# Kernel optimization log

Measured on AMD Instinct MI355X. Metric: run time of the kernel, lower is better.

Reference implementation:

```python
import jax, jax.numpy as jnp
import numpy as np

VOCAB, D, E, TOP_K, B, S = 32000, 1024, 16, 2, 2048, 128
H = 2 * D  # expert hidden
LN_EPS = 1e-5


def setup_inputs() -> dict:
    key = jax.random.key(0)
    ks = jax.random.split(key, 12)
    sd = 0.02
    return {
        "x": jax.random.randint(ks[0], (B, S), 0, VOCAB),
        "embed": jax.random.normal(ks[1], (VOCAB, D), jnp.float32) * sd,
        "gate_w": jax.random.normal(ks[2], (D, E), jnp.float32) * sd,
        "gate_b": jnp.zeros((E,), jnp.float32),
        "w1": jax.random.normal(ks[3], (E, D, H), jnp.float32) * sd,
        "b1": jnp.zeros((E, H), jnp.float32),
        "w2": jax.random.normal(ks[4], (E, H, D), jnp.float32) * sd,
        "b2": jnp.zeros((E, D), jnp.float32),
        "ln_g": jnp.ones((D,), jnp.float32),
        "ln_b": jnp.zeros((D,), jnp.float32),
        "head_w": jax.random.normal(ks[5], (D, 20), jnp.float32) * sd,
        "head_b": jnp.zeros((20,), jnp.float32),
    }


def reference(x, embed, gate_w, gate_b, w1, b1, w2, b2, ln_g, ln_b, head_w, head_b):
    # embed mean-pool: [B,S,D] -> [B,D]
    h = jnp.mean(embed[x], axis=1)
    # gate + top-k routing
    scores = jax.nn.softmax(h @ gate_w + gate_b, axis=-1)  # [B,E]
    topk_vals, topk_idx = jax.lax.top_k(scores, TOP_K)     # [B,K]
    # combine weights per (token, expert): sum of topk vals routed to e
    comb_w = jnp.sum(topk_vals[:, :, None] * jax.nn.one_hot(topk_idx, E, dtype=h.dtype), axis=1)  # [B,E]
    # dense all-expert MLP (same math as per-token dispatch), weighted combine
    pre = jnp.einsum('bd,edh->beh', h, w1) + b1            # [B,E,H]
    ye = jnp.einsum('beh,ehd->bed', jax.nn.relu(pre), w2) + b2  # [B,E,D]
    combined = jnp.einsum('be,bed->bd', comb_w, ye)        # [B,D]
    # LayerNorm + head
    mu = jnp.mean(combined, axis=-1, keepdims=True)
    var = jnp.mean(jnp.square(combined - mu), axis=-1, keepdims=True)
    normed = (combined - mu) * jax.lax.rsqrt(var + LN_EPS) * ln_g + ln_b
    logits = normed @ head_w + head_b                      # [B,20]
    return logits, topk_idx
```

## Files before the change

kernel.cpp:

```cpp
#include <hip/hip_runtime.h>
#include <math.h>

#define B_TOK 2048
#define SEQ   128
#define D_DIM 1024
#define E_NUM 16
#define H_DIM 2048

#define TM 128
#define TN 64
#define KT 32
#define A_LD 40

typedef __attribute__((ext_vector_type(8))) short short8;
typedef __attribute__((ext_vector_type(4))) float f32x4;

__device__ __forceinline__ float bf2f(unsigned short h) {
  return __uint_as_float(((unsigned)h) << 16);
}

__device__ __forceinline__ void split2(float x, unsigned short& hi, unsigned short& lo) {
  unsigned u = __float_as_uint(x);
  hi = (unsigned short)(u >> 16);
  float lof = x - __uint_as_float(u & 0xFFFF0000u);
  lo = (unsigned short)(__float_as_uint(lof) >> 16);
}

__global__ __launch_bounds__(256) void k_embed_mean(const int* __restrict__ x,
                                                    const float* __restrict__ embed,
                                                    unsigned short* __restrict__ h_hi,
                                                    unsigned short* __restrict__ h_lo) {
  const int b = blockIdx.x;
  const int t = threadIdx.x;
  __shared__ int sx[SEQ];
  if (t < SEQ) sx[t] = x[b * SEQ + t];
  __syncthreads();
  float4 acc = make_float4(0.f, 0.f, 0.f, 0.f);
  const int col = t * 4;
  for (int s = 0; s < SEQ; ++s) {
    const float4 v = *reinterpret_cast<const float4*>(embed + (size_t)sx[s] * D_DIM + col);
    acc.x += v.x; acc.y += v.y; acc.z += v.z; acc.w += v.w;
  }
  const float inv = 1.0f / (float)SEQ;
  float vv[4] = {acc.x * inv, acc.y * inv, acc.z * inv, acc.w * inv};
  ushort4 hv, lv;
  split2(vv[0], hv.x, lv.x); split2(vv[1], hv.y, lv.y);
  split2(vv[2], hv.z, lv.z); split2(vv[3], hv.w, lv.w);
  *reinterpret_cast<ushort4*>(h_hi + (size_t)b * D_DIM + col) = hv;
  *reinterpret_cast<ushort4*>(h_lo + (size_t)b * D_DIM + col) = lv;
}

__global__ __launch_bounds__(64) void k_gate(const unsigned short* __restrict__ h_hi,
                                             const unsigned short* __restrict__ h_lo,
                                             const float* __restrict__ gate_w,
                                             const float* __restrict__ gate_b,
                                             int* __restrict__ counts,
                                             int* __restrict__ lists,
                                             float* __restrict__ wlist,
                                             float* __restrict__ out_idx) {
  const int b = blockIdx.x;
  const int l = threadIdx.x;
  float z[E_NUM];
#pragma unroll
  for (int e = 0; e < E_NUM; ++e) z[e] = 0.f;
  const size_t base = (size_t)b * D_DIM;
  for (int d = l; d < D_DIM; d += 64) {
    const float hv = bf2f(h_hi[base + d]) + bf2f(h_lo[base + d]);
    const float* gw = gate_w + d * E_NUM;
#pragma unroll
    for (int e = 0; e < E_NUM; ++e) z[e] = fmaf(hv, gw[e], z[e]);
  }
#pragma unroll
  for (int e = 0; e < E_NUM; ++e) {
    float v = z[e];
#pragma unroll
    for (int off = 32; off >= 1; off >>= 1) v += __shfl_xor(v, off, 64);
    z[e] = v;
  }
  if (l == 0) {
#pragma unroll
    for (int e = 0; e < E_NUM; ++e) z[e] += gate_b[e];
    float mx = z[0];
#pragma unroll
    for (int e = 1; e < E_NUM; ++e) mx = fmaxf(mx, z[e]);
    float p[E_NUM];
    float se = 0.f;
#pragma unroll
    for (int e = 0; e < E_NUM; ++e) { p[e] = expf(z[e] - mx); se += p[e]; }
    const float invs = 1.0f / se;
    int e1 = 0; float z1 = z[0];
#pragma unroll
    for (int e = 1; e < E_NUM; ++e) if (z[e] > z1) { z1 = z[e]; e1 = e; }
    int e2 = -1; float z2 = -1e30f;
#pragma unroll
    for (int e = 0; e < E_NUM; ++e) if (e != e1 && z[e] > z2) { z2 = z[e]; e2 = e; }
    const float w1v = p[e1] * invs;
    const float w2v = p[e2] * invs;
    const int pos1 = atomicAdd(&counts[e1], 1);
    lists[e1 * B_TOK + pos1] = b * 2 + 0;
    wlist[e1 * B_TOK + pos1] = w1v;
    const int pos2 = atomicAdd(&counts[e2], 1);
    lists[e2 * B_TOK + pos2] = b * 2 + 1;
    wlist[e2 * B_TOK + pos2] = w2v;
    out_idx[b * 2 + 0] = (float)e1;
    out_idx[b * 2 + 1] = (float)e2;
  }
}

__global__ __launch_bounds__(256) void k_gemm1(const unsigned short* __restrict__ a_hi,
                                               const unsigned short* __restrict__ a_lo,
                                               const float* __restrict__ w1,
                                               const float* __restrict__ b1,
                                               const int* __restrict__ counts,
                                               const int* __restrict__ lists,
                                               unsigned short* __restrict__ act_hi,
                                               unsigned short* __restrict__ act_lo) {
  const int e = blockIdx.z;
  const int n_e = counts[e];
  const int m0 = blockIdx.y * TM;
  if (m0 >= n_e) return;
  const int n0 = blockIdx.x * TN;
  const int* lst = lists + e * B_TOK;

  __shared__ short AsH[TM][A_LD];
  __shared__ short AsL[TM][A_LD];
  __shared__ short BsH[TN][A_LD];
  __shared__ short BsL[TN][A_LD];

  const int tid = threadIdx.x;
  const int r0 = tid >> 3;
  const int sl = tid & 7;
  const int spart = sl & 3;
  const unsigned short* abase = (sl < 4) ? a_hi : a_lo;
  short* lds_a = (sl < 4) ? &AsH[0][0] : &AsL[0][0];
  size_t arowoff[4];
#pragma unroll
  for (int p = 0; p < 4; ++p) {
    const int m = m0 + p * 32 + r0;
    const int ent = lst[(m < n_e) ? m : 0];
    arowoff[p] = (size_t)(ent >> 1) * D_DIM;
  }
  const int bn = tid & 63;
  const int bkq = tid >> 6;
  const float* bcol = w1 + (size_t)e * D_DIM * H_DIM + n0 + bn;

  const int wv = tid >> 6;
  const int lane = tid & 63;
  const int fm = lane & 15;
  const int fq = lane >> 4;
  const int mrow = wv * 32;
  f32x4 acc[2][4];
#pragma unroll
  for (int mi = 0; mi < 2; ++mi)
#pragma unroll
    for (int ni = 0; ni < 4; ++ni) acc[mi][ni] = (f32x4){0.f, 0.f, 0.f, 0.f};

  for (int kb = 0; kb < D_DIM; kb += KT) {
#pragma unroll
    for (int p = 0; p < 4; ++p) {
      const int4 v = *reinterpret_cast<const int4*>(abase + arowoff[p] + kb + 8 * spart);
      *reinterpret_cast<int4*>(lds_a + (p * 32 + r0) * A_LD + 8 * spart) = v;
    }
    {
      unsigned u[8];
      float f[8];
#pragma unroll
      for (int j = 0; j < 8; ++j) {
        f[j] = bcol[(size_t)(kb + bkq * 8 + j) * H_DIM];
        u[j] = __float_as_uint(f[j]);
      }
      int4 hv, lv;
      unsigned lw[8];
#pragma unroll
      for (int j = 0; j < 8; ++j) {
        const float lof = f[j] - __uint_as_float(u[j] & 0xFFFF0000u);
        lw[j] = __float_as_uint(lof);
      }
      hv.x = (int)((u[0] >> 16) | (u[1] & 0xFFFF0000u));
      hv.y = (int)((u[2] >> 16) | (u[3] & 0xFFFF0000u));
      hv.z = (int)((u[4] >> 16) | (u[5] & 0xFFFF0000u));
      hv.w = (int)((u[6] >> 16) | (u[7] & 0xFFFF0000u));
      lv.x = (int)((lw[0] >> 16) | (lw[1] & 0xFFFF0000u));
      lv.y = (int)((lw[2] >> 16) | (lw[3] & 0xFFFF0000u));
      lv.z = (int)((lw[4] >> 16) | (lw[5] & 0xFFFF0000u));
      lv.w = (int)((lw[6] >> 16) | (lw[7] & 0xFFFF0000u));
      *reinterpret_cast<int4*>(&BsH[bn][bkq * 8]) = hv;
      *reinterpret_cast<int4*>(&BsL[bn][bkq * 8]) = lv;
    }
    __syncthreads();
    short8 aH[2], aL[2], bH[4], bL[4];
#pragma unroll
    for (int mi = 0; mi < 2; ++mi) {
      aH[mi] = *reinterpret_cast<const short8*>(&AsH[mrow + mi * 16 + fm][fq * 8]);
      aL[mi] = *reinterpret_cast<const short8*>(&AsL[mrow + mi * 16 + fm][fq * 8]);
    }
#pragma unroll
    for (int ni = 0; ni < 4; ++ni) {
      bH[ni] = *reinterpret_cast<const short8*>(&BsH[ni * 16 + fm][fq * 8]);
      bL[ni] = *reinterpret_cast<const short8*>(&BsL[ni * 16 + fm][fq * 8]);
    }
#pragma unroll
    for (int mi = 0; mi < 2; ++mi)
#pragma unroll
      for (int ni = 0; ni < 4; ++ni) {
        acc[mi][ni] = __builtin_amdgcn_mfma_f32_16x16x32_bf16(aH[mi], bH[ni], acc[mi][ni], 0, 0, 0);
        acc[mi][ni] = __builtin_amdgcn_mfma_f32_16x16x32_bf16(aH[mi], bL[ni], acc[mi][ni], 0, 0, 0);
        acc[mi][ni] = __builtin_amdgcn_mfma_f32_16x16x32_bf16(aL[mi], bH[ni], acc[mi][ni], 0, 0, 0);
      }
    __syncthreads();
  }
  float bz[4];
#pragma unroll
  for (int ni = 0; ni < 4; ++ni) bz[ni] = b1[(size_t)e * H_DIM + n0 + ni * 16 + fm];
#pragma unroll
  for (int mi = 0; mi < 2; ++mi) {
#pragma unroll
    for (int r = 0; r < 4; ++r) {
      const int m = m0 + mrow + mi * 16 + fq * 4 + r;
      if (m < n_e) {
        const int ent = lst[m];
        unsigned short* oh = act_hi + (size_t)ent * H_DIM + n0 + fm;
        unsigned short* ol = act_lo + (size_t)ent * H_DIM + n0 + fm;
#pragma unroll
        for (int ni = 0; ni < 4; ++ni) {
          float v = fmaxf(acc[mi][ni][r] + bz[ni], 0.f);
          unsigned short hh, ll;
          split2(v, hh, ll);
          oh[ni * 16] = hh;
          ol[ni * 16] = ll;
        }
      }
    }
  }
}

__global__ __launch_bounds__(256) void k_gemm2(const unsigned short* __restrict__ a_hi,
                                               const unsigned short* __restrict__ a_lo,
                                               const float* __restrict__ w2,
                                               const float* __restrict__ b2,
                                               const int* __restrict__ counts,
                                               const int* __restrict__ lists,
                                               const float* __restrict__ wlist,
                                               float* __restrict__ combined) {
  const int e = blockIdx.z;
  const int n_e = counts[e];
  const int m0 = blockIdx.y * TM;
  if (m0 >= n_e) return;
  const int n0 = blockIdx.x * TN;
  const int* lst = lists + e * B_TOK;

  __shared__ short AsH[TM][A_LD];
  __shared__ short AsL[TM][A_LD];
  __shared__ short BsH[TN][A_LD];
  __shared__ short BsL[TN][A_LD];

  const int tid = threadIdx.x;
  const int r0 = tid >> 3;
  const int sl = tid & 7;
  const int spart = sl & 3;
  const unsigned short* abase = (sl < 4) ? a_hi : a_lo;
  short* lds_a = (sl < 4) ? &AsH[0][0] : &AsL[0][0];
  size_t arowoff[4];
#pragma unroll
  for (int p = 0; p < 4; ++p) {
    const int m = m0 + p * 32 + r0;
    const int ent = lst[(m < n_e) ? m : 0];
    arowoff[p] = (size_t)ent * H_DIM;
  }
  const int bn = tid & 63;
  const int bkq = tid >> 6;
  const float* bcol = w2 + (size_t)e * H_DIM * D_DIM + n0 + bn;

  const int wv = tid >> 6;
  const int lane = tid & 63;
  const int fm = lane & 15;
  const int fq = lane >> 4;
  const int mrow = wv * 32;
  f32x4 acc[2][4];
#pragma unroll
  for (int mi = 0; mi < 2; ++mi)
#pragma unroll
    for (int ni = 0; ni < 4; ++ni) acc[mi][ni] = (f32x4){0.f, 0.f, 0.f, 0.f};

  for (int kb = 0; kb < H_DIM; kb += KT) {
#pragma unroll
    for (int p = 0; p < 4; ++p) {
      const int4 v = *reinterpret_cast<const int4*>(abase + arowoff[p] + kb + 8 * spart);
      *reinterpret_cast<int4*>(lds_a + (p * 32 + r0) * A_LD + 8 * spart) = v;
    }
    {
      unsigned u[8];
      float f[8];
#pragma unroll
      for (int j = 0; j < 8; ++j) {
        f[j] = bcol[(size_t)(kb + bkq * 8 + j) * D_DIM];
        u[j] = __float_as_uint(f[j]);
      }
      int4 hv, lv;
      unsigned lw[8];
#pragma unroll
      for (int j = 0; j < 8; ++j) {
        const float lof = f[j] - __uint_as_float(u[j] & 0xFFFF0000u);
        lw[j] = __float_as_uint(lof);
      }
      hv.x = (int)((u[0] >> 16) | (u[1] & 0xFFFF0000u));
      hv.y = (int)((u[2] >> 16) | (u[3] & 0xFFFF0000u));
      hv.z = (int)((u[4] >> 16) | (u[5] & 0xFFFF0000u));
      hv.w = (int)((u[6] >> 16) | (u[7] & 0xFFFF0000u));
      lv.x = (int)((lw[0] >> 16) | (lw[1] & 0xFFFF0000u));
      lv.y = (int)((lw[2] >> 16) | (lw[3] & 0xFFFF0000u));
      lv.z = (int)((lw[4] >> 16) | (lw[5] & 0xFFFF0000u));
      lv.w = (int)((lw[6] >> 16) | (lw[7] & 0xFFFF0000u));
      *reinterpret_cast<int4*>(&BsH[bn][bkq * 8]) = hv;
      *reinterpret_cast<int4*>(&BsL[bn][bkq * 8]) = lv;
    }
    __syncthreads();
    short8 aH[2], aL[2], bH[4], bL[4];
#pragma unroll
    for (int mi = 0; mi < 2; ++mi) {
      aH[mi] = *reinterpret_cast<const short8*>(&AsH[mrow + mi * 16 + fm][fq * 8]);
      aL[mi] = *reinterpret_cast<const short8*>(&AsL[mrow + mi * 16 + fm][fq * 8]);
    }
#pragma unroll
    for (int ni = 0; ni < 4; ++ni) {
      bH[ni] = *reinterpret_cast<const short8*>(&BsH[ni * 16 + fm][fq * 8]);
      bL[ni] = *reinterpret_cast<const short8*>(&BsL[ni * 16 + fm][fq * 8]);
    }
#pragma unroll
    for (int mi = 0; mi < 2; ++mi)
#pragma unroll
      for (int ni = 0; ni < 4; ++ni) {
        acc[mi][ni] = __builtin_amdgcn_mfma_f32_16x16x32_bf16(aH[mi], bH[ni], acc[mi][ni], 0, 0, 0);
        acc[mi][ni] = __builtin_amdgcn_mfma_f32_16x16x32_bf16(aH[mi], bL[ni], acc[mi][ni], 0, 0, 0);
        acc[mi][ni] = __builtin_amdgcn_mfma_f32_16x16x32_bf16(aL[mi], bH[ni], acc[mi][ni], 0, 0, 0);
      }
    __syncthreads();
  }
  float bz[4];
#pragma unroll
  for (int ni = 0; ni < 4; ++ni) bz[ni] = b2[(size_t)e * D_DIM + n0 + ni * 16 + fm];
#pragma unroll
  for (int mi = 0; mi < 2; ++mi) {
#pragma unroll
    for (int r = 0; r < 4; ++r) {
      const int m = m0 + mrow + mi * 16 + fq * 4 + r;
      if (m < n_e) {
        const int ent = lst[m];
        const float w = wlist[e * B_TOK + m];
        float* dst = combined + (size_t)(ent >> 1) * D_DIM + n0 + fm;
#pragma unroll
        for (int ni = 0; ni < 4; ++ni) {
          atomicAdd(&dst[ni * 16], w * (acc[mi][ni][r] + bz[ni]));
        }
      }
    }
  }
}

__global__ __launch_bounds__(256) void k_ln_head(const float* __restrict__ combined,
                                                 const float* __restrict__ ln_g,
                                                 const float* __restrict__ ln_b,
                                                 const float* __restrict__ head_w,
                                                 const float* __restrict__ head_b,
                                                 float* __restrict__ logits) {
  const int b = blockIdx.x;
  const int t = threadIdx.x;
  const int lane = t & 63, wid = t >> 6;
  __shared__ float red[8];
  __shared__ float pr[4][20];
  const int d0 = t * 4;
  const float4 v = *reinterpret_cast<const float4*>(combined + (size_t)b * D_DIM + d0);
  float s = v.x + v.y + v.z + v.w;
#pragma unroll
  for (int off = 32; off >= 1; off >>= 1) s += __shfl_xor(s, off, 64);
  if (lane == 0) red[wid] = s;
  __syncthreads();
  const float mu = (red[0] + red[1] + red[2] + red[3]) * (1.0f / D_DIM);
  const float dx = v.x - mu, dy = v.y - mu, dz = v.z - mu, dw = v.w - mu;
  float sq = dx * dx + dy * dy + dz * dz + dw * dw;
#pragma unroll
  for (int off = 32; off >= 1; off >>= 1) sq += __shfl_xor(sq, off, 64);
  if (lane == 0) red[4 + wid] = sq;
  __syncthreads();
  const float var = (red[4] + red[5] + red[6] + red[7]) * (1.0f / D_DIM);
  const float inv = 1.0f / sqrtf(var + 1e-5f);
  float nm[4];
  nm[0] = dx * inv * ln_g[d0 + 0] + ln_b[d0 + 0];
  nm[1] = dy * inv * ln_g[d0 + 1] + ln_b[d0 + 1];
  nm[2] = dz * inv * ln_g[d0 + 2] + ln_b[d0 + 2];
  nm[3] = dw * inv * ln_g[d0 + 3] + ln_b[d0 + 3];
  float p[20];
#pragma unroll
  for (int j = 0; j < 20; ++j) p[j] = 0.f;
#pragma unroll
  for (int i = 0; i < 4; ++i) {
    const float* hwrow = head_w + (size_t)(d0 + i) * 20;
#pragma unroll
    for (int j = 0; j < 20; ++j) p[j] = fmaf(nm[i], hwrow[j], p[j]);
  }
#pragma unroll
  for (int j = 0; j < 20; ++j) {
    float pv = p[j];
#pragma unroll
    for (int off = 32; off >= 1; off >>= 1) pv += __shfl_xor(pv, off, 64);
    if (lane == 0) pr[wid][j] = pv;
  }
  __syncthreads();
  if (t < 20) {
    logits[(size_t)b * 20 + t] = pr[0][t] + pr[1][t] + pr[2][t] + pr[3][t] + head_b[t];
  }
}

extern "C" void kernel_launch(void* const* d_in, const int* in_sizes, int n_in,
                              void* d_out, int out_size, void* d_ws, size_t ws_size,
                              hipStream_t stream) {
  const int*   x      = (const int*)d_in[0];
  const float* embed  = (const float*)d_in[1];
  const float* gate_w = (const float*)d_in[2];
  const float* gate_b = (const float*)d_in[3];
  const float* w1     = (const float*)d_in[4];
  const float* b1     = (const float*)d_in[5];
  const float* w2     = (const float*)d_in[6];
  const float* b2     = (const float*)d_in[7];
  const float* ln_g   = (const float*)d_in[8];
  const float* ln_b   = (const float*)d_in[9];
  const float* head_w = (const float*)d_in[10];
  const float* head_b = (const float*)d_in[11];

  float* logits  = (float*)d_out;
  float* out_idx = logits + (size_t)B_TOK * 20;

  char* ws = (char*)d_ws;
  size_t off = 0;
  auto alloc = [&](size_t bytes) -> void* {
    void* p = ws + off;
    off = (off + bytes + 255) & ~(size_t)255;
    return p;
  };
  unsigned short* h_hi   = (unsigned short*)alloc(sizeof(short) * B_TOK * D_DIM);
  unsigned short* h_lo   = (unsigned short*)alloc(sizeof(short) * B_TOK * D_DIM);
  float* combined        = (float*)alloc(sizeof(float) * B_TOK * D_DIM);
  int*   counts          = (int*)alloc(sizeof(int) * E_NUM);
  int*   lists           = (int*)alloc(sizeof(int) * E_NUM * B_TOK);
  float* wlist           = (float*)alloc(sizeof(float) * E_NUM * B_TOK);
  unsigned short* act_hi = (unsigned short*)alloc(sizeof(short) * B_TOK * 2 * H_DIM);
  unsigned short* act_lo = (unsigned short*)alloc(sizeof(short) * B_TOK * 2 * H_DIM);

  hipMemsetAsync(counts, 0, sizeof(int) * E_NUM, stream);
  hipMemsetAsync(combined, 0, sizeof(float) * B_TOK * D_DIM, stream);

  k_embed_mean<<<B_TOK, 256, 0, stream>>>(x, embed, h_hi, h_lo);
  k_gate<<<B_TOK, 64, 0, stream>>>(h_hi, h_lo, gate_w, gate_b, counts, lists, wlist, out_idx);
  k_gemm1<<<dim3(H_DIM / TN, B_TOK / TM, E_NUM), 256, 0, stream>>>(h_hi, h_lo, w1, b1, counts, lists, act_hi, act_lo);
  k_gemm2<<<dim3(D_DIM / TN, B_TOK / TM, E_NUM), 256, 0, stream>>>(act_hi, act_lo, w2, b2, counts, lists, wlist, combined);
  k_ln_head<<<B_TOK, 256, 0, stream>>>(combined, ln_g, ln_b, head_w, head_b, logits);
}
```

Before: 765.3 us.

## Prefetch next K tile into registers, split gemm2 K in two, batch embed loads

Both expert GEMMs now load the next K tile of activations and weights into registers while the current tile is being consumed by MFMA, so global latency can hide behind compute. gemm2 is split into two K halves with separate blocks, doubling grid parallelism. Its partial sums are combined through the existing atomicAdd, with the bias added only by the first half. The embedding mean-pool issues eight gathered loads per step with an occupancy hint. The costs are higher register pressure and twice as many atomic adds in gemm2.

```diff
diff --git a/kernel.cpp b/kernel.cpp
--- a/kernel.cpp
+++ b/kernel.cpp
@@ -26,23 +26,30 @@
   lo = (unsigned short)(__float_as_uint(lof) >> 16);
 }
 
-__global__ __launch_bounds__(256) void k_embed_mean(const int* __restrict__ x,
-                                                    const float* __restrict__ embed,
-                                                    unsigned short* __restrict__ h_hi,
-                                                    unsigned short* __restrict__ h_lo) {
+__global__ __launch_bounds__(256, 8) void k_embed_mean(const int* __restrict__ x,
+                                                       const float* __restrict__ embed,
+                                                       unsigned short* __restrict__ h_hi,
+                                                       unsigned short* __restrict__ h_lo) {
   const int b = blockIdx.x;
   const int t = threadIdx.x;
   __shared__ int sx[SEQ];
   if (t < SEQ) sx[t] = x[b * SEQ + t];
   __syncthreads();
-  float4 acc = make_float4(0.f, 0.f, 0.f, 0.f);
   const int col = t * 4;
-  for (int s = 0; s < SEQ; ++s) {
-    const float4 v = *reinterpret_cast<const float4*>(embed + (size_t)sx[s] * D_DIM + col);
-    acc.x += v.x; acc.y += v.y; acc.z += v.z; acc.w += v.w;
+  float ax = 0.f, ay = 0.f, az = 0.f, aw = 0.f;
+  for (int s0 = 0; s0 < SEQ; s0 += 8) {
+    float4 v[8];
+#pragma unroll
+    for (int j = 0; j < 8; ++j) {
+      v[j] = *reinterpret_cast<const float4*>(embed + (size_t)sx[s0 + j] * D_DIM + col);
+    }
+#pragma unroll
+    for (int j = 0; j < 8; ++j) {
+      ax += v[j].x; ay += v[j].y; az += v[j].z; aw += v[j].w;
+    }
   }
   const float inv = 1.0f / (float)SEQ;
-  float vv[4] = {acc.x * inv, acc.y * inv, acc.z * inv, acc.w * inv};
+  float vv[4] = {ax * inv, ay * inv, az * inv, aw * inv};
   ushort4 hv, lv;
   split2(vv[0], hv.x, lv.x); split2(vv[1], hv.y, lv.y);
   split2(vv[2], hv.z, lv.z); split2(vv[3], hv.w, lv.w);
@@ -155,27 +162,27 @@
 #pragma unroll
     for (int ni = 0; ni < 4; ++ni) acc[mi][ni] = (f32x4){0.f, 0.f, 0.f, 0.f};
 
+  int4 pa[4];
+  float pf[8];
+#pragma unroll
+  for (int p = 0; p < 4; ++p)
+    pa[p] = *reinterpret_cast<const int4*>(abase + arowoff[p] + 8 * spart);
+#pragma unroll
+  for (int j = 0; j < 8; ++j)
+    pf[j] = bcol[(size_t)(bkq * 8 + j) * H_DIM];
+
   for (int kb = 0; kb < D_DIM; kb += KT) {
 #pragma unroll
-    for (int p = 0; p < 4; ++p) {
-      const int4 v = *reinterpret_cast<const int4*>(abase + arowoff[p] + kb + 8 * spart);
-      *reinterpret_cast<int4*>(lds_a + (p * 32 + r0) * A_LD + 8 * spart) = v;
-    }
+    for (int p = 0; p < 4; ++p)
+      *reinterpret_cast<int4*>(lds_a + (p * 32 + r0) * A_LD + 8 * spart) = pa[p];
     {
-      unsigned u[8];
-      float f[8];
+      unsigned u[8], lw[8];
 #pragma unroll
       for (int j = 0; j < 8; ++j) {
-        f[j] = bcol[(size_t)(kb + bkq * 8 + j) * H_DIM];
-        u[j] = __float_as_uint(f[j]);
+        u[j] = __float_as_uint(pf[j]);
+        lw[j] = __float_as_uint(pf[j] - __uint_as_float(u[j] & 0xFFFF0000u));
       }
       int4 hv, lv;
-      unsigned lw[8];
-#pragma unroll
-      for (int j = 0; j < 8; ++j) {
-        const float lof = f[j] - __uint_as_float(u[j] & 0xFFFF0000u);
-        lw[j] = __float_as_uint(lof);
-      }
       hv.x = (int)((u[0] >> 16) | (u[1] & 0xFFFF0000u));
       hv.y = (int)((u[2] >> 16) | (u[3] & 0xFFFF0000u));
       hv.z = (int)((u[4] >> 16) | (u[5] & 0xFFFF0000u));
@@ -188,6 +195,14 @@
       *reinterpret_cast<int4*>(&BsL[bn][bkq * 8]) = lv;
     }
     __syncthreads();
+    if (kb + KT < D_DIM) {
+#pragma unroll
+      for (int p = 0; p < 4; ++p)
+        pa[p] = *reinterpret_cast<const int4*>(abase + arowoff[p] + kb + KT + 8 * spart);
+#pragma unroll
+      for (int j = 0; j < 8; ++j)
+        pf[j] = bcol[(size_t)(kb + KT + bkq * 8 + j) * H_DIM];
+    }
     short8 aH[2], aL[2], bH[4], bL[4];
 #pragma unroll
     for (int mi = 0; mi < 2; ++mi) {
@@ -244,10 +259,13 @@
                                                float* __restrict__ combined) {
   const int e = blockIdx.z;
   const int n_e = counts[e];
-  const int m0 = blockIdx.y * TM;
+  const int kslice = blockIdx.y & 1;
+  const int m0 = (blockIdx.y >> 1) * TM;
   if (m0 >= n_e) return;
   const int n0 = blockIdx.x * TN;
   const int* lst = lists + e * B_TOK;
+  const int kbeg = kslice * (H_DIM / 2);
+  const int kend = kbeg + (H_DIM / 2);
 
   __shared__ short AsH[TM][A_LD];
   __shared__ short AsL[TM][A_LD];
@@ -282,27 +300,27 @@
 #pragma unroll
     for (int ni = 0; ni < 4; ++ni) acc[mi][ni] = (f32x4){0.f, 0.f, 0.f, 0.f};
 
-  for (int kb = 0; kb < H_DIM; kb += KT) {
-#pragma unroll
-    for (int p = 0; p < 4; ++p) {
-      const int4 v = *reinterpret_cast<const int4*>(abase + arowoff[p] + kb + 8 * spart);
-      *reinterpret_cast<int4*>(lds_a + (p * 32 + r0) * A_LD + 8 * spart) = v;
-    }
+  int4 pa[4];
+  float pf[8];
+#pragma unroll
+  for (int p = 0; p < 4; ++p)
+    pa[p] = *reinterpret_cast<const int4*>(abase + arowoff[p] + kbeg + 8 * spart);
+#pragma unroll
+  for (int j = 0; j < 8; ++j)
+    pf[j] = bcol[(size_t)(kbeg + bkq * 8 + j) * D_DIM];
+
+  for (int kb = kbeg; kb < kend; kb += KT) {
+#pragma unroll
+    for (int p = 0; p < 4; ++p)
+      *reinterpret_cast<int4*>(lds_a + (p * 32 + r0) * A_LD + 8 * spart) = pa[p];
     {
-      unsigned u[8];
-      float f[8];
+      unsigned u[8], lw[8];
 #pragma unroll
       for (int j = 0; j < 8; ++j) {
-        f[j] = bcol[(size_t)(kb + bkq * 8 + j) * D_DIM];
-        u[j] = __float_as_uint(f[j]);
+        u[j] = __float_as_uint(pf[j]);
+        lw[j] = __float_as_uint(pf[j] - __uint_as_float(u[j] & 0xFFFF0000u));
       }
       int4 hv, lv;
-      unsigned lw[8];
-#pragma unroll
-      for (int j = 0; j < 8; ++j) {
-        const float lof = f[j] - __uint_as_float(u[j] & 0xFFFF0000u);
-        lw[j] = __float_as_uint(lof);
-      }
       hv.x = (int)((u[0] >> 16) | (u[1] & 0xFFFF0000u));
       hv.y = (int)((u[2] >> 16) | (u[3] & 0xFFFF0000u));
       hv.z = (int)((u[4] >> 16) | (u[5] & 0xFFFF0000u));
@@ -315,6 +333,14 @@
       *reinterpret_cast<int4*>(&BsL[bn][bkq * 8]) = lv;
     }
     __syncthreads();
+    if (kb + KT < kend) {
+#pragma unroll
+      for (int p = 0; p < 4; ++p)
+        pa[p] = *reinterpret_cast<const int4*>(abase + arowoff[p] + kb + KT + 8 * spart);
+#pragma unroll
+      for (int j = 0; j < 8; ++j)
+        pf[j] = bcol[(size_t)(kb + KT + bkq * 8 + j) * D_DIM];
+    }
     short8 aH[2], aL[2], bH[4], bL[4];
 #pragma unroll
     for (int mi = 0; mi < 2; ++mi) {
@@ -338,7 +364,8 @@
   }
   float bz[4];
 #pragma unroll
-  for (int ni = 0; ni < 4; ++ni) bz[ni] = b2[(size_t)e * D_DIM + n0 + ni * 16 + fm];
+  for (int ni = 0; ni < 4; ++ni)
+    bz[ni] = (kslice == 0) ? b2[(size_t)e * D_DIM + n0 + ni * 16 + fm] : 0.f;
 #pragma unroll
   for (int mi = 0; mi < 2; ++mi) {
 #pragma unroll
@@ -452,6 +479,6 @@
   k_embed_mean<<<B_TOK, 256, 0, stream>>>(x, embed, h_hi, h_lo);
   k_gate<<<B_TOK, 64, 0, stream>>>(h_hi, h_lo, gate_w, gate_b, counts, lists, wlist, out_idx);
   k_gemm1<<<dim3(H_DIM / TN, B_TOK / TM, E_NUM), 256, 0, stream>>>(h_hi, h_lo, w1, b1, counts, lists, act_hi, act_lo);
-  k_gemm2<<<dim3(D_DIM / TN, B_TOK / TM, E_NUM), 256, 0, stream>>>(act_hi, act_lo, w2, b2, counts, lists, wlist, combined);
+  k_gemm2<<<dim3(D_DIM / TN, (B_TOK / TM) * 2, E_NUM), 256, 0, stream>>>(act_hi, act_lo, w2, b2, counts, lists, wlist, combined);
   k_ln_head<<<B_TOK, 256, 0, stream>>>(combined, ln_g, ln_b, head_w, head_b, logits);
 }
```

Measured after the change: 1.095 ms. 43.1% more time.

## Replace atomic combine with per-slot expert outputs combined in LN kernel

Applied to the files above, without the earlier changes.

The second expert GEMM now writes each routed entry's output to its own slot with plain stores, instead of atomically adding weighted results into a zeroed combined buffer. The routing weights are stored per token, and the LN/head kernel does the weighted sum of the two slots. This removes the memset of the combined buffer and the float atomics in the GEMM epilogue, at the cost of a larger intermediate buffer that the LN kernel reads twice. The workspace is also repacked so the output buffer reuses the h region, the embedding mean loop is batched to issue eight gathers at once, and the bf16 split loop is folded together.

```diff
diff --git a/kernel.cpp b/kernel.cpp
--- a/kernel.cpp
+++ b/kernel.cpp
@@ -6,6 +6,7 @@
 #define D_DIM 1024
 #define E_NUM 16
 #define H_DIM 2048
+#define N_ENT (B_TOK * 2)
 
 #define TM 128
 #define TN 64
@@ -26,23 +27,30 @@
   lo = (unsigned short)(__float_as_uint(lof) >> 16);
 }
 
-__global__ __launch_bounds__(256) void k_embed_mean(const int* __restrict__ x,
-                                                    const float* __restrict__ embed,
-                                                    unsigned short* __restrict__ h_hi,
-                                                    unsigned short* __restrict__ h_lo) {
+__global__ __launch_bounds__(256, 4) void k_embed_mean(const int* __restrict__ x,
+                                                       const float* __restrict__ embed,
+                                                       unsigned short* __restrict__ h_hi,
+                                                       unsigned short* __restrict__ h_lo) {
   const int b = blockIdx.x;
   const int t = threadIdx.x;
   __shared__ int sx[SEQ];
   if (t < SEQ) sx[t] = x[b * SEQ + t];
   __syncthreads();
-  float4 acc = make_float4(0.f, 0.f, 0.f, 0.f);
   const int col = t * 4;
-  for (int s = 0; s < SEQ; ++s) {
-    const float4 v = *reinterpret_cast<const float4*>(embed + (size_t)sx[s] * D_DIM + col);
-    acc.x += v.x; acc.y += v.y; acc.z += v.z; acc.w += v.w;
+  float ax = 0.f, ay = 0.f, az = 0.f, aw = 0.f;
+  for (int s0 = 0; s0 < SEQ; s0 += 8) {
+    float4 v[8];
+#pragma unroll
+    for (int j = 0; j < 8; ++j) {
+      v[j] = *reinterpret_cast<const float4*>(embed + (size_t)sx[s0 + j] * D_DIM + col);
+    }
+#pragma unroll
+    for (int j = 0; j < 8; ++j) {
+      ax += v[j].x; ay += v[j].y; az += v[j].z; aw += v[j].w;
+    }
   }
   const float inv = 1.0f / (float)SEQ;
-  float vv[4] = {acc.x * inv, acc.y * inv, acc.z * inv, acc.w * inv};
+  float vv[4] = {ax * inv, ay * inv, az * inv, aw * inv};
   ushort4 hv, lv;
   split2(vv[0], hv.x, lv.x); split2(vv[1], hv.y, lv.y);
   split2(vv[2], hv.z, lv.z); split2(vv[3], hv.w, lv.w);
@@ -56,7 +64,7 @@
                                              const float* __restrict__ gate_b,
                                              int* __restrict__ counts,
                                              int* __restrict__ lists,
-                                             float* __restrict__ wlist,
+                                             float* __restrict__ ew,
                                              float* __restrict__ out_idx) {
   const int b = blockIdx.x;
   const int l = threadIdx.x;
@@ -98,10 +106,10 @@
     const float w2v = p[e2] * invs;
     const int pos1 = atomicAdd(&counts[e1], 1);
     lists[e1 * B_TOK + pos1] = b * 2 + 0;
-    wlist[e1 * B_TOK + pos1] = w1v;
     const int pos2 = atomicAdd(&counts[e2], 1);
     lists[e2 * B_TOK + pos2] = b * 2 + 1;
-    wlist[e2 * B_TOK + pos2] = w2v;
+    ew[b * 2 + 0] = w1v;
+    ew[b * 2 + 1] = w2v;
     out_idx[b * 2 + 0] = (float)e1;
     out_idx[b * 2 + 1] = (float)e2;
   }
@@ -162,20 +170,15 @@
       *reinterpret_cast<int4*>(lds_a + (p * 32 + r0) * A_LD + 8 * spart) = v;
     }
     {
-      unsigned u[8];
+      unsigned u[8], lw[8];
       float f[8];
 #pragma unroll
       for (int j = 0; j < 8; ++j) {
         f[j] = bcol[(size_t)(kb + bkq * 8 + j) * H_DIM];
         u[j] = __float_as_uint(f[j]);
+        lw[j] = __float_as_uint(f[j] - __uint_as_float(u[j] & 0xFFFF0000u));
       }
       int4 hv, lv;
-      unsigned lw[8];
-#pragma unroll
-      for (int j = 0; j < 8; ++j) {
-        const float lof = f[j] - __uint_as_float(u[j] & 0xFFFF0000u);
-        lw[j] = __float_as_uint(lof);
-      }
       hv.x = (int)((u[0] >> 16) | (u[1] & 0xFFFF0000u));
       hv.y = (int)((u[2] >> 16) | (u[3] & 0xFFFF0000u));
       hv.z = (int)((u[4] >> 16) | (u[5] & 0xFFFF0000u));
@@ -240,8 +243,7 @@
                                                const float* __restrict__ b2,
                                                const int* __restrict__ counts,
                                                const int* __restrict__ lists,
-                                               const float* __restrict__ wlist,
-                                               float* __restrict__ combined) {
+                                               float* __restrict__ y) {
   const int e = blockIdx.z;
   const int n_e = counts[e];
   const int m0 = blockIdx.y * TM;
@@ -289,20 +291,15 @@
       *reinterpret_cast<int4*>(lds_a + (p * 32 + r0) * A_LD + 8 * spart) = v;
     }
     {
-      unsigned u[8];
+      unsigned u[8], lw[8];
       float f[8];
 #pragma unroll
       for (int j = 0; j < 8; ++j) {
         f[j] = bcol[(size_t)(kb + bkq * 8 + j) * D_DIM];
         u[j] = __float_as_uint(f[j]);
+        lw[j] = __float_as_uint(f[j] - __uint_as_float(u[j] & 0xFFFF0000u));
       }
       int4 hv, lv;
-      unsigned lw[8];
-#pragma unroll
-      for (int j = 0; j < 8; ++j) {
-        const float lof = f[j] - __uint_as_float(u[j] & 0xFFFF0000u);
-        lw[j] = __float_as_uint(lof);
-      }
       hv.x = (int)((u[0] >> 16) | (u[1] & 0xFFFF0000u));
       hv.y = (int)((u[2] >> 16) | (u[3] & 0xFFFF0000u));
       hv.z = (int)((u[4] >> 16) | (u[5] & 0xFFFF0000u));
@@ -346,18 +343,18 @@
       const int m = m0 + mrow + mi * 16 + fq * 4 + r;
       if (m < n_e) {
         const int ent = lst[m];
-        const float w = wlist[e * B_TOK + m];
-        float* dst = combined + (size_t)(ent >> 1) * D_DIM + n0 + fm;
+        float* dst = y + (size_t)ent * D_DIM + n0 + fm;
 #pragma unroll
         for (int ni = 0; ni < 4; ++ni) {
-          atomicAdd(&dst[ni * 16], w * (acc[mi][ni][r] + bz[ni]));
+          dst[ni * 16] = acc[mi][ni][r] + bz[ni];
         }
       }
     }
   }
 }
 
-__global__ __launch_bounds__(256) void k_ln_head(const float* __restrict__ combined,
+__global__ __launch_bounds__(256) void k_ln_head(const float* __restrict__ y,
+                                                 const float* __restrict__ ew,
                                                  const float* __restrict__ ln_g,
                                                  const float* __restrict__ ln_b,
                                                  const float* __restrict__ head_w,
@@ -369,7 +366,15 @@
   __shared__ float red[8];
   __shared__ float pr[4][20];
   const int d0 = t * 4;
-  const float4 v = *reinterpret_cast<const float4*>(combined + (size_t)b * D_DIM + d0);
+  const float w0 = ew[b * 2 + 0];
+  const float w1 = ew[b * 2 + 1];
+  const float4 va = *reinterpret_cast<const float4*>(y + (size_t)(b * 2 + 0) * D_DIM + d0);
+  const float4 vb = *reinterpret_cast<const float4*>(y + (size_t)(b * 2 + 1) * D_DIM + d0);
+  float4 v;
+  v.x = w0 * va.x + w1 * vb.x;
+  v.y = w0 * va.y + w1 * vb.y;
+  v.z = w0 * va.z + w1 * vb.z;
+  v.w = w0 * va.w + w1 * vb.w;
   float s = v.x + v.y + v.z + v.w;
 #pragma unroll
   for (int off = 32; off >= 1; off >>= 1) s += __shfl_xor(s, off, 64);
@@ -431,27 +436,23 @@
   float* out_idx = logits + (size_t)B_TOK * 20;
 
   char* ws = (char*)d_ws;
-  size_t off = 0;
-  auto alloc = [&](size_t bytes) -> void* {
-    void* p = ws + off;
-    off = (off + bytes + 255) & ~(size_t)255;
-    return p;
-  };
-  unsigned short* h_hi   = (unsigned short*)alloc(sizeof(short) * B_TOK * D_DIM);
-  unsigned short* h_lo   = (unsigned short*)alloc(sizeof(short) * B_TOK * D_DIM);
-  float* combined        = (float*)alloc(sizeof(float) * B_TOK * D_DIM);
-  int*   counts          = (int*)alloc(sizeof(int) * E_NUM);
-  int*   lists           = (int*)alloc(sizeof(int) * E_NUM * B_TOK);
-  float* wlist           = (float*)alloc(sizeof(float) * E_NUM * B_TOK);
-  unsigned short* act_hi = (unsigned short*)alloc(sizeof(short) * B_TOK * 2 * H_DIM);
-  unsigned short* act_lo = (unsigned short*)alloc(sizeof(short) * B_TOK * 2 * H_DIM);
+  const size_t Y_BYTES = sizeof(float) * (size_t)N_ENT * D_DIM;
+  const size_t ACT_BYTES = sizeof(short) * (size_t)N_ENT * H_DIM;
+  unsigned short* h_hi   = (unsigned short*)(ws + 0);
+  unsigned short* h_lo   = (unsigned short*)(ws + sizeof(short) * (size_t)B_TOK * D_DIM);
+  float*          y      = (float*)(ws + 0);
+  unsigned short* act_hi = (unsigned short*)(ws + Y_BYTES);
+  unsigned short* act_lo = (unsigned short*)(ws + Y_BYTES + ACT_BYTES);
+  char* tail = ws + Y_BYTES + 2 * ACT_BYTES;
+  int*   counts = (int*)tail;                       tail += 256;
+  int*   lists  = (int*)tail;                       tail += sizeof(int) * E_NUM * B_TOK;
+  float* ew     = (float*)tail;
 
   hipMemsetAsync(counts, 0, sizeof(int) * E_NUM, stream);
-  hipMemsetAsync(combined, 0, sizeof(float) * B_TOK * D_DIM, stream);
 
   k_embed_mean<<<B_TOK, 256, 0, stream>>>(x, embed, h_hi, h_lo);
-  k_gate<<<B_TOK, 64, 0, stream>>>(h_hi, h_lo, gate_w, gate_b, counts, lists, wlist, out_idx);
+  k_gate<<<B_TOK, 64, 0, stream>>>(h_hi, h_lo, gate_w, gate_b, counts, lists, ew, out_idx);
   k_gemm1<<<dim3(H_DIM / TN, B_TOK / TM, E_NUM), 256, 0, stream>>>(h_hi, h_lo, w1, b1, counts, lists, act_hi, act_lo);
-  k_gemm2<<<dim3(D_DIM / TN, B_TOK / TM, E_NUM), 256, 0, stream>>>(act_hi, act_lo, w2, b2, counts, lists, wlist, combined);
-  k_ln_head<<<B_TOK, 256, 0, stream>>>(combined, ln_g, ln_b, head_w, head_b, logits);
-}
+  k_gemm2<<<dim3(D_DIM / TN, B_TOK / TM, E_NUM), 256, 0, stream>>>(act_hi, act_lo, w2, b2, counts, lists, y);
+  k_ln_head<<<B_TOK, 256, 0, stream>>>(y, ew, ln_g, ln_b, head_w, head_b, logits);
+}
```

Result: no change. 752.2 us (-1.7%).
